# Kernel optimization log

Measured on AMD Instinct MI355X. Metric: run time of the kernel, lower is better.

## Reference

```python
import jax, jax.numpy as jnp
import numpy as np


def _pad_kernel_like(kernel_oc0, H, W, ks):
    # torch: F.pad(k,(p,p,p,p)) then if shape mismatch F.pad(k,(0,1,0,1))
    p = (H - ks) // 2
    extra = H - (ks + 2 * p)  # 0 or 1
    return jnp.pad(kernel_oc0, ((0, 0), (p, p + extra), (p, p + extra)))


def setup_inputs() -> dict:
    key = jax.random.key(0)
    k1, k2 = jax.random.split(key)
    B, C, H, W = 8, 16, 128, 128
    O, KS = 32, 9
    x = jax.random.normal(k1, (B, C, H, W), dtype=jnp.float32)
    # kaiming_uniform-ish init scale
    fan_in = C * KS * KS
    bound = float(np.sqrt(6.0 / fan_in))
    kernel = jax.random.uniform(k2, (O, C, KS, KS), dtype=jnp.float32,
                                minval=-bound, maxval=bound)
    return {"x": x, "kernel": kernel}


def reference(x, kernel):
    # x: [B,C,H,W] float32, kernel: [O,C,ks,ks] float32
    B, C, H, W = x.shape
    O, ks = kernel.shape[0], kernel.shape[-1]
    # Faithful to original bug: only kernel[:, 0] is used for every input channel.
    k = _pad_kernel_like(kernel[:, 0], H, W, ks)  # [O,H,W]
    # 4f optical FFT convolution: ifftshift -> FFT -> multiply -> IFFT -> fftshift -> |.|
    Fx = jnp.fft.fft2(jnp.fft.ifftshift(x, axes=(-2, -1)))   # [B,C,H,W] complex64
    Fk = jnp.fft.fft2(jnp.fft.ifftshift(k, axes=(-2, -1)))   # [O,H,W]   complex64
    prod = Fx[:, None, :, :, :] * Fk[None, :, None, :, :]    # [B,O,C,H,W]
    field = jnp.fft.fftshift(jnp.fft.ifft2(prod), axes=(-2, -1))
    out_pc = jnp.abs(field)                                  # per-(out,in)-channel intensity
    return out_pc.sum(axis=2)                                # [B,O,H,W]
```

## Files before the change

kernel.cpp:

```cpp
#include <hip/hip_runtime.h>


typedef __attribute__((ext_vector_type(8)))  short  short8;
typedef __attribute__((ext_vector_type(16))) float  float16v;
typedef __attribute__((ext_vector_type(4)))  float  float4v;
typedef __attribute__((ext_vector_type(4)))  unsigned int uint4v;

#define XR_ROWS 138
#define XR_RDW  72
#define XR_CH_DW (XR_ROWS * XR_RDW)
#define XR_CH_B  (XR_CH_DW * 4)
#define BPRE_OFF ((size_t)128 * XR_ROWS * 288)
#define CHB 3168

__device__ __forceinline__ unsigned int f2bf(float f) {
    union { float f; unsigned int u; } a; a.f = f;
    unsigned int u = a.u;
    u += 0x7fffu + ((u >> 16) & 1u);
    return u >> 16;
}

#if __has_builtin(__builtin_amdgcn_alignbit)
#define ALIGN16(hi_, lo_) __builtin_amdgcn_alignbit((hi_), (lo_), 16)
#else
#define ALIGN16(hi_, lo_) \
    (unsigned int)((((unsigned long long)(hi_) << 32) | (lo_)) >> 16)
#endif

#define FRAG_EVEN(q_) __builtin_bit_cast(short8, (uint4v){                    \
        wnd[(q_)+0], wnd[(q_)+1], wnd[(q_)+2], wnd[(q_)+3]})
#define FRAG_ODD(q_)  __builtin_bit_cast(short8, (uint4v){                    \
        ALIGN16(wnd[(q_)+1], wnd[(q_)+0]),                                    \
        ALIGN16(wnd[(q_)+2], wnd[(q_)+1]),                                    \
        ALIGN16(wnd[(q_)+3], wnd[(q_)+2]),                                    \
        ALIGN16(wnd[(q_)+4], wnd[(q_)+3])})

__device__ __forceinline__ void gload_lds16(const void* g, void* l) {
    __builtin_amdgcn_global_load_lds(
        (const __attribute__((address_space(1))) unsigned int*)g,
        (__attribute__((address_space(3))) unsigned int*)l, 16, 0, 0);
}

__global__ __launch_bounds__(256)
void optical_prep_69698729279498(const float* __restrict__ x,
                                 const float* __restrict__ kern,
                                 unsigned int* __restrict__ xr,
                                 uint4v* __restrict__ bpre) {
    const int t = blockIdx.x * 256 + threadIdx.x;
    const int bc = blockIdx.y;
    const int rem = t - 9984;
    if (t < XR_CH_DW) {
        int r   = t / 72;
        int ccd = t - r * 72;
        int cc  = 2 * ccd;
        const float* xp = x + (bc << 14) + ((r & 127) << 7);
        float v0 = xp[(132 - cc) & 127];
        float v1 = xp[(131 - cc) & 127];
        xr[(size_t)bc * XR_CH_DW + t] = f2bf(v0) | (f2bf(v1) << 16);
    } else if (bc == 0 && rem >= 0 && rem < 64) {
        const int l  = rem;
        const int o  = l & 31;
        const int hi = l >> 5;
        for (int ti = 0; ti < 9; ++ti) {
            unsigned int pk[4];
#pragma unroll
            for (int ee = 0; ee < 4; ++ee) {
                int tj_a = 8 * hi + 2 * ee, tj_b = tj_a + 1;
                float va = (tj_a <= 8) ? kern[o * 1296 + ti * 9 + tj_a] : 0.f;
                float vb = (tj_b <= 8) ? kern[o * 1296 + ti * 9 + tj_b] : 0.f;
                pk[ee] = f2bf(va) | (f2bf(vb) << 16);
            }
            bpre[ti * 64 + l] = (uint4v){pk[0], pk[1], pk[2], pk[3]};
        }
    }
}

__global__ __launch_bounds__(256, 2)
void optical_conv_69698729279498(const unsigned int* __restrict__ xr,
                                 const uint4v* __restrict__ bpre,
                                 float* __restrict__ out) {
    __shared__ __align__(16) unsigned short ldsb[16 * (CHB / 2)];

    const int tid = threadIdx.x;
    const int l   = tid & 63;
    const int w   = tid >> 6;
    const int ph  = w & 1;
    const int cg  = w >> 1;
    const int i0  = blockIdx.x * 2;
    const int b   = blockIdx.y;

    const int jm  = l & 15;
    const int rl  = (l >> 4) & 1;
    const int hi  = l >> 5;

    const int wstart = (i0 >= 4) ? (i0 - 4) : (i0 + 124);
    const char* xr8 = (const char*)xr;
#pragma unroll
    for (int cw = 0; cw < 4; ++cw) {
        const int ch = 4 * w + cw;
        const char* src = xr8 + ((size_t)((b * 16 + ch) * XR_ROWS + wstart)) * 288;
        char* dst = (char*)ldsb + ch * CHB;
        gload_lds16(src + 0 * 1024 + l * 16, dst + 0 * 1024);
        gload_lds16(src + 1 * 1024 + l * 16, dst + 1 * 1024);
        gload_lds16(src + 2 * 1024 + l * 16, dst + 2 * 1024);
        if (l < 6)
            gload_lds16(src + 3072 + l * 16, dst + 3072);
    }

    short8 Bf[9];
#pragma unroll
    for (int ti = 0; ti < 9; ++ti)
        Bf[ti] = __builtin_bit_cast(short8, bpre[ti * 64 + l]);

    __syncthreads();

    float16v acc[4];
#pragma unroll
    for (int pp = 0; pp < 4; ++pp)
#pragma unroll
        for (int e = 0; e < 16; ++e) acc[pp][e] = 0.f;
    float16v zero16;
#pragma unroll
    for (int e = 0; e < 16; ++e) zero16[e] = 0.f;

    const char* lb = (const char*)ldsb
                   + (240 - 16 * jm + 16 * hi) + (1 + rl) * 288
                   + cg * 8 * CHB;

    for (int c = 0; c < 8; ++c) {
        float16v D[4];
#pragma unroll
        for (int ti = 0; ti < 9; ++ti) {
            const char* p = lb + (8 - ti) * 288;
            uint4v w0 = *(const uint4v*)p;
            uint4v w1 = *(const uint4v*)(p + 16);
            unsigned int wnd[8] = {w0.x, w0.y, w0.z, w0.w,
                                   w1.x, w1.y, w1.z, w1.w};
            short8 f0, f1, f2, f3;
            if (ph == 0) {
                f0 = FRAG_ODD(3);  f1 = FRAG_EVEN(3);
                f2 = FRAG_ODD(2);  f3 = FRAG_EVEN(2);
            } else {
                f0 = FRAG_ODD(1);  f1 = FRAG_EVEN(1);
                f2 = FRAG_ODD(0);  f3 = FRAG_EVEN(0);
            }
            D[0] = __builtin_amdgcn_mfma_f32_32x32x16_bf16(f0, Bf[ti], ti ? D[0] : zero16, 0, 0, 0);
            D[1] = __builtin_amdgcn_mfma_f32_32x32x16_bf16(f1, Bf[ti], ti ? D[1] : zero16, 0, 0, 0);
            D[2] = __builtin_amdgcn_mfma_f32_32x32x16_bf16(f2, Bf[ti], ti ? D[2] : zero16, 0, 0, 0);
            D[3] = __builtin_amdgcn_mfma_f32_32x32x16_bf16(f3, Bf[ti], ti ? D[3] : zero16, 0, 0, 0);
        }
#pragma unroll
        for (int pp = 0; pp < 4; ++pp)
#pragma unroll
            for (int e = 0; e < 16; ++e) acc[pp][e] += fabsf(D[pp][e]);
        lb += CHB;
    }

    __syncthreads();
    float* otile = (float*)ldsb;
    const int obase_l = (l & 31) * 129 + 32 * (l >> 5) + 4 * ph;
    if (cg == 1) {
#pragma unroll
        for (int pp = 0; pp < 4; ++pp)
#pragma unroll
            for (int reg = 0; reg < 16; ++reg)
                otile[obase_l + (reg >> 3) * 4128 + 8 * (reg & 3)
                      + 64 * ((reg >> 2) & 1) + pp] = acc[pp][reg];
    }
    __syncthreads();
    if (cg == 0) {
#pragma unroll
        for (int pp = 0; pp < 4; ++pp)
#pragma unroll
            for (int reg = 0; reg < 16; ++reg) {
                const int idx = obase_l + (reg >> 3) * 4128 + 8 * (reg & 3)
                              + 64 * ((reg >> 2) & 1) + pp;
                otile[idx] += acc[pp][reg];
            }
    }
    __syncthreads();

    {
        const int pair = l;
        const int q    = w;
        const int r    = pair >> 5;
        const int o    = pair & 31;
        const float* src = otile + pair * 129 + q * 32;
        float* dstg = out + ((((size_t)(b * 32 + o)) * 128 + (i0 + r)) << 7) + q * 32;
#pragma unroll
        for (int k4 = 0; k4 < 8; ++k4) {
            float4v v = (float4v){src[4 * k4], src[4 * k4 + 1],
                                  src[4 * k4 + 2], src[4 * k4 + 3]};
            *(float4v*)&dstg[4 * k4] = v;
        }
    }
}

extern "C" void kernel_launch(void* const* d_in, const int* in_sizes, int n_in,
                              void* d_out, int out_size, void* d_ws, size_t ws_size,
                              hipStream_t stream) {
    const float* x = (const float*)d_in[0];
    const float* kern = (const float*)d_in[1];
    float* out = (float*)d_out;
    unsigned int* xr = (unsigned int*)d_ws;
    uint4v* bpre = (uint4v*)((char*)d_ws + BPRE_OFF);

    hipLaunchKernelGGL(optical_prep_69698729279498, dim3(40, 128),
                       dim3(256), 0, stream, x, kern, xr, bpre);
    hipLaunchKernelGGL(optical_conv_69698729279498, dim3(64, 8), dim3(256),
                       0, stream, xr, bpre, out);
}
```

Measured before the change: 95.23 us.

## Fuse bf16 prep into conv kernel, loading and packing x and kernel in-block

Removes the separate prep kernel and its workspace. Each conv block now reads float x directly from global, applies the shift and bf16 packing, and writes the result into LDS. It also stages the 9x9 kernel taps into LDS and builds the MFMA B fragments per wave. This drops one launch and the round trip through the workspace. In exchange the rows are redundantly converted across neighbouring blocks, global loads become scattered scalar reads instead of async global_load_lds, and LDS use grows, which may cut occupancy.

```diff
diff --git a/kernel.cpp b/kernel.cpp
--- a/kernel.cpp
+++ b/kernel.cpp
@@ -6,11 +6,6 @@
 typedef __attribute__((ext_vector_type(4)))  float  float4v;
 typedef __attribute__((ext_vector_type(4)))  unsigned int uint4v;
 
-#define XR_ROWS 138
-#define XR_RDW  72
-#define XR_CH_DW (XR_ROWS * XR_RDW)
-#define XR_CH_B  (XR_CH_DW * 4)
-#define BPRE_OFF ((size_t)128 * XR_ROWS * 288)
 #define CHB 3168
 
 __device__ __forceinline__ unsigned int f2bf(float f) {
@@ -35,51 +30,11 @@
         ALIGN16(wnd[(q_)+3], wnd[(q_)+2]),                                    \
         ALIGN16(wnd[(q_)+4], wnd[(q_)+3])})
 
-__device__ __forceinline__ void gload_lds16(const void* g, void* l) {
-    __builtin_amdgcn_global_load_lds(
-        (const __attribute__((address_space(1))) unsigned int*)g,
-        (__attribute__((address_space(3))) unsigned int*)l, 16, 0, 0);
-}
-
-__global__ __launch_bounds__(256)
-void optical_prep_69698729279498(const float* __restrict__ x,
-                                 const float* __restrict__ kern,
-                                 unsigned int* __restrict__ xr,
-                                 uint4v* __restrict__ bpre) {
-    const int t = blockIdx.x * 256 + threadIdx.x;
-    const int bc = blockIdx.y;
-    const int rem = t - 9984;
-    if (t < XR_CH_DW) {
-        int r   = t / 72;
-        int ccd = t - r * 72;
-        int cc  = 2 * ccd;
-        const float* xp = x + (bc << 14) + ((r & 127) << 7);
-        float v0 = xp[(132 - cc) & 127];
-        float v1 = xp[(131 - cc) & 127];
-        xr[(size_t)bc * XR_CH_DW + t] = f2bf(v0) | (f2bf(v1) << 16);
-    } else if (bc == 0 && rem >= 0 && rem < 64) {
-        const int l  = rem;
-        const int o  = l & 31;
-        const int hi = l >> 5;
-        for (int ti = 0; ti < 9; ++ti) {
-            unsigned int pk[4];
-#pragma unroll
-            for (int ee = 0; ee < 4; ++ee) {
-                int tj_a = 8 * hi + 2 * ee, tj_b = tj_a + 1;
-                float va = (tj_a <= 8) ? kern[o * 1296 + ti * 9 + tj_a] : 0.f;
-                float vb = (tj_b <= 8) ? kern[o * 1296 + ti * 9 + tj_b] : 0.f;
-                pk[ee] = f2bf(va) | (f2bf(vb) << 16);
-            }
-            bpre[ti * 64 + l] = (uint4v){pk[0], pk[1], pk[2], pk[3]};
-        }
-    }
-}
-
 __global__ __launch_bounds__(256, 2)
-void optical_conv_69698729279498(const unsigned int* __restrict__ xr,
-                                 const uint4v* __restrict__ bpre,
-                                 float* __restrict__ out) {
-    __shared__ __align__(16) unsigned short ldsb[16 * (CHB / 2)];
+void optical_fused_69698729279498(const float* __restrict__ x,
+                                  const float* __restrict__ kern,
+                                  float* __restrict__ out) {
+    __shared__ __align__(16) unsigned short ldsb[25344 + 5184];
 
     const int tid = threadIdx.x;
     const int l   = tid & 63;
@@ -93,26 +48,63 @@
     const int rl  = (l >> 4) & 1;
     const int hi  = l >> 5;
 
-    const int wstart = (i0 >= 4) ? (i0 - 4) : (i0 + 124);
-    const char* xr8 = (const char*)xr;
-#pragma unroll
-    for (int cw = 0; cw < 4; ++cw) {
-        const int ch = 4 * w + cw;
-        const char* src = xr8 + ((size_t)((b * 16 + ch) * XR_ROWS + wstart)) * 288;
-        char* dst = (char*)ldsb + ch * CHB;
-        gload_lds16(src + 0 * 1024 + l * 16, dst + 0 * 1024);
-        gload_lds16(src + 1 * 1024 + l * 16, dst + 1 * 1024);
-        gload_lds16(src + 2 * 1024 + l * 16, dst + 2 * 1024);
-        if (l < 6)
-            gload_lds16(src + 3072 + l * 16, dst + 3072);
-    }
+    unsigned int* ldsx = (unsigned int*)ldsb;
+    float* kldsf = (float*)(ldsb + 25344);
+
+    {
+        const float* xb = x + ((size_t)b << 18);
+        int d    = tid % 72;
+        int rw   = tid / 72;
+        int ch   = 0;
+        int ldsi = tid + 72;
+        const int gb = i0 + 125;
+#pragma unroll 5
+        for (int k = 0; k < 45; ++k) {
+            const int grow = (gb + rw) & 127;
+            const float* xp = xb + (ch << 14) + (grow << 7);
+            const int c0 = (132 - 2 * d) & 127;
+            const int c1 = (131 - 2 * d) & 127;
+            ldsx[ldsi] = f2bf(xp[c0]) | (f2bf(xp[c1]) << 16);
+            d += 40; if (d >= 72) { d -= 72; rw += 1; }
+            rw += 3; ldsi += 256;
+            if (rw >= 10) { rw -= 10; ch += 1; ldsi += 72; }
+        }
+    }
+
+    {
+#pragma unroll
+        for (int k = 0; k < 10; ++k) {
+            const int v = tid + (k << 8);
+            const int o = v / 81;
+            kldsf[v] = kern[o * 1296 + (v - o * 81)];
+        }
+        if (tid < 32) {
+            const int v = 2560 + tid;
+            const int o = v / 81;
+            kldsf[v] = kern[o * 1296 + (v - o * 81)];
+        }
+    }
+
+    __syncthreads();
 
     short8 Bf[9];
-#pragma unroll
-    for (int ti = 0; ti < 9; ++ti)
-        Bf[ti] = __builtin_bit_cast(short8, bpre[ti * 64 + l]);
-
-    __syncthreads();
+    {
+        const int o  = l & 31;
+        const int kb = l >> 5;
+        const float* kp = kldsf + o * 81;
+#pragma unroll
+        for (int ti = 0; ti < 9; ++ti) {
+            unsigned int pk[4];
+#pragma unroll
+            for (int ee = 0; ee < 4; ++ee) {
+                const int tj_a = 8 * kb + 2 * ee, tj_b = tj_a + 1;
+                const float va = (tj_a <= 8) ? kp[ti * 9 + tj_a] : 0.f;
+                const float vb = (tj_b <= 8) ? kp[ti * 9 + tj_b] : 0.f;
+                pk[ee] = f2bf(va) | (f2bf(vb) << 16);
+            }
+            Bf[ti] = __builtin_bit_cast(short8, (uint4v){pk[0], pk[1], pk[2], pk[3]});
+        }
+    }
 
     float16v acc[4];
 #pragma unroll
@@ -199,14 +191,11 @@
 extern "C" void kernel_launch(void* const* d_in, const int* in_sizes, int n_in,
                               void* d_out, int out_size, void* d_ws, size_t ws_size,
                               hipStream_t stream) {
+    (void)in_sizes; (void)n_in; (void)d_ws; (void)ws_size; (void)out_size;
     const float* x = (const float*)d_in[0];
     const float* kern = (const float*)d_in[1];
     float* out = (float*)d_out;
-    unsigned int* xr = (unsigned int*)d_ws;
-    uint4v* bpre = (uint4v*)((char*)d_ws + BPRE_OFF);
-
-    hipLaunchKernelGGL(optical_prep_69698729279498, dim3(40, 128),
-                       dim3(256), 0, stream, x, kern, xr, bpre);
-    hipLaunchKernelGGL(optical_conv_69698729279498, dim3(64, 8), dim3(256),
-                       0, stream, xr, bpre, out);
+
+    hipLaunchKernelGGL(optical_fused_69698729279498, dim3(64, 8), dim3(256),
+                       0, stream, x, kern, out);
 }
```

Result: no change. 94.09 us (-1.2%).
